# Kernel tuning notes

Measured on AMD Instinct MI355X. Metric: run time of the kernel, lower is better.

## Reference

```python
import jax, jax.numpy as jnp
import numpy as np

B, S, E, A = 4, 2048, 1024, 1024


def setup_inputs() -> dict:
    key = jax.random.key(0)
    k0, k1, k2, k3 = jax.random.split(key, 4)
    scale = 1.0 / np.sqrt(E)
    return {
        "embeds": jax.random.normal(k0, (B, S, E), dtype=jnp.float32),
        "Wq": jax.random.normal(k1, (E, A), dtype=jnp.float32) * scale,
        "Wk": jax.random.normal(k2, (E, A), dtype=jnp.float32) * scale,
        "Wv": jax.random.normal(k3, (E, A), dtype=jnp.float32) * scale,
    }


def reference(embeds, Wq, Wk, Wv):
    # projections: [B, S, A]
    q = jnp.einsum("bse,ea->bsa", embeds, Wq)
    k = jnp.einsum("bse,ea->bsa", embeds, Wk)
    v = jnp.einsum("bse,ea->bsa", embeds, Wv)
    attn_dim = k.shape[-1]
    # scores: [B, S, S], scaled by sqrt(attention_dim)
    scores = jnp.einsum("bqa,bka->bqk", q, k) / jnp.sqrt(
        jnp.asarray(attn_dim, dtype=q.dtype)
    )
    seq = scores.shape[-1]
    causal = jnp.tril(jnp.ones((seq, seq), dtype=bool))  # [S, S]
    scores = jnp.where(causal[None, :, :], scores, -jnp.inf)
    probs = jax.nn.softmax(scores, axis=-1)
    return jnp.einsum("bqk,bka->bqa", probs, v)
```

## Files before the change

kernel.cpp:

```cpp
#include <hip/hip_runtime.h>
#include <hip/hip_bf16.h>

#define DI __device__ __forceinline__

typedef __attribute__((ext_vector_type(8))) __bf16 bf16x8;
typedef __attribute__((ext_vector_type(4))) float f32x4;
typedef __attribute__((ext_vector_type(8))) short short8;
typedef __attribute__((ext_vector_type(4))) short short4v;
typedef unsigned short u16;

static constexpr int BB = 4, SS = 2048, EE = 1024, AA = 1024;

DI float bf2f(u16 u) { unsigned v = ((unsigned)u) << 16; float f; __builtin_memcpy(&f, &v, 4); return f; }
DI u16 f2bf(float f) { __hip_bfloat16 h = __float2bfloat16(f); u16 u; __builtin_memcpy(&u, &h, 2); return u; }

DI void gload16(const void* g, void* l) {
  __builtin_amdgcn_global_load_lds((const __attribute__((address_space(1))) void*)g,
                                   (__attribute__((address_space(3))) void*)l, 16, 0, 0);
}

DI int xcd_swz(int lin, int nwg) {
  int cpx = nwg >> 3;
  return (lin & 7) * cpx + (lin >> 3);
}

DI bf16x8 read_frag(const char* lds, int R, int c) {
  return *(const bf16x8*)(lds + R * 128 + ((c ^ (R & 7)) << 4));
}

DI void stage_tile(const u16* g, int ld, char* lds, int wid, int lane) {
#pragma unroll
  for (int i = 0; i < 4; ++i) {
    int blk = i * 4 + wid;
    int r = blk * 8 + (lane >> 3);
    int c = (lane & 7) ^ (r & 7);
    gload16((const char*)(g + (size_t)r * ld) + c * 16, lds + blk * 1024);
  }
}

DI void gemm_tile(const u16* Ap, int lda, const u16* Bp, int ldb, int ksteps,
                  char* smem, f32x4 acc[4][4]) {
  const int tid = threadIdx.x, lane = tid & 63, wid = tid >> 6;
  const int wr = wid >> 1, wc = wid & 1;
  stage_tile(Ap, lda, smem, wid, lane);
  stage_tile(Bp, ldb, smem + 16384, wid, lane);
  asm volatile("s_waitcnt vmcnt(0)" ::: "memory");
  __syncthreads();
#pragma unroll 1
  for (int ks = 0; ks < ksteps; ++ks) {
    const char* As = smem + (ks & 1) * 32768;
    const char* Bs = As + 16384;
    char* nxt = smem + ((ks & 1) ^ 1) * 32768;
    if (ks + 1 < ksteps) {
      stage_tile(Ap + (size_t)(ks + 1) * 64, lda, nxt, wid, lane);
      stage_tile(Bp + (size_t)(ks + 1) * 64, ldb, nxt + 16384, wid, lane);
    }
#pragma unroll
    for (int ksub = 0; ksub < 2; ++ksub) {
      const int c = ksub * 4 + (lane >> 4);
      bf16x8 af[4], bfr[4];
#pragma unroll
      for (int mi = 0; mi < 4; ++mi) af[mi] = read_frag(As, wr * 64 + mi * 16 + (lane & 15), c);
#pragma unroll
      for (int ni = 0; ni < 4; ++ni) bfr[ni] = read_frag(Bs, wc * 64 + ni * 16 + (lane & 15), c);
#pragma unroll
      for (int mi = 0; mi < 4; ++mi)
#pragma unroll
        for (int ni = 0; ni < 4; ++ni)
          acc[mi][ni] = __builtin_amdgcn_mfma_f32_16x16x32_bf16(af[mi], bfr[ni], acc[mi][ni], 0, 0, 0);
    }
    if (ks + 1 < ksteps) asm volatile("s_waitcnt vmcnt(0)" ::: "memory");
    __syncthreads();
  }
}

__global__ __launch_bounds__(256) void k_proj8(const u16* __restrict__ Xb, const u16* __restrict__ Wt,
                                               u16* __restrict__ Qb, u16* __restrict__ Vt) {
  __shared__ __align__(16) char smem[65536];
  const int lin = blockIdx.x;
  const int x = lin & 7;
  const int jj = lin >> 3;
  const int nh = jj / 96, rem = jj - nh * 96;
  const int nt = nh * 12 + (rem >> 3);
  const int mt = x * 8 + (rem & 7);
  const u16* Ap = Xb + (size_t)mt * 128 * EE;
  const u16* Bp = Wt + (size_t)nt * 128 * EE;
  f32x4 acc[4][4];
#pragma unroll
  for (int p = 0; p < 4; ++p)
#pragma unroll
    for (int q = 0; q < 4; ++q) acc[p][q] = (f32x4)0.f;
  gemm_tile(Ap, EE, Bp, EE, EE / 64, smem, acc);

  const int lane = threadIdx.x & 63, wid = threadIdx.x >> 6;
  const int lane15 = lane & 15, lhi = lane >> 4;
  const int wr = wid >> 1, wc = wid & 1;
  const int r0 = mt * 128 + wr * 64;
  const int c0 = nt * 128 + wc * 64;
  if (nt < 16) {
    u16* base = Qb + (size_t)(nt >> 3) * ((size_t)BB * SS * AA);
    const int cc = c0 & 1023;
#pragma unroll
    for (int mi = 0; mi < 4; ++mi)
#pragma unroll
      for (int ni = 0; ni < 4; ++ni)
#pragma unroll
        for (int r = 0; r < 4; ++r) {
          int row = r0 + mi * 16 + lhi * 4 + r;
          base[(size_t)row * AA + cc + ni * 16 + lane15] = f2bf(acc[mi][ni][r]);
        }
  } else {
#pragma unroll
    for (int mi = 0; mi < 4; ++mi) {
      const int grow = r0 + mi * 16 + lhi * 4;
      const int b = grow >> 11, s = grow & 2047;
#pragma unroll
      for (int ni = 0; ni < 4; ++ni) {
        const int a = c0 - 2048 + ni * 16 + lane15;
        short4v o;
#pragma unroll
        for (int r = 0; r < 4; ++r) o[r] = (short)f2bf(acc[mi][ni][r]);
        *(short4v*)(Vt + (size_t)b * AA * SS + (size_t)a * SS + s) = o;
      }
    }
  }
}

__global__ __launch_bounds__(256) void k_prep(const float* __restrict__ X, const float* __restrict__ Wq,
                                              const float* __restrict__ Wk, const float* __restrict__ Wv,
                                              u16* __restrict__ Xb, u16* __restrict__ Wt,
                                              float* __restrict__ rowsum) {
  __shared__ float t[64][65];
  const int bid = blockIdx.x;
  if (bid < 8192) {
    if (bid < 32) rowsum[bid * 256 + threadIdx.x] = 0.f;
    size_t i = ((size_t)bid * 256 + threadIdx.x) * 4;
    f32x4 f = *(const f32x4*)(X + i);
    short4v o;
#pragma unroll
    for (int j = 0; j < 4; ++j) o[j] = (short)f2bf(f[j]);
    *(short4v*)(Xb + i) = o;
  } else {
    const int bx = bid - 8192;
    const int w = bx >> 8, rem = bx & 255;
    const int k0 = (rem & 15) * 64, n0 = (rem >> 4) * 64;
    const float* W = (w == 0) ? Wq : ((w == 1) ? Wk : Wv);
    u16* Wo = Wt + (size_t)w * EE * AA;
    const int tx = threadIdx.x & 63, ty = threadIdx.x >> 6;
#pragma unroll
    for (int r = 0; r < 16; ++r) {
      int k = r * 4 + ty;
      t[k][tx] = W[(size_t)(k0 + k) * AA + n0 + tx];
    }
    __syncthreads();
#pragma unroll
    for (int r = 0; r < 16; ++r) {
      int n = r * 4 + ty;
      Wo[(size_t)(n0 + n) * EE + k0 + tx] = f2bf(t[tx][n]);
    }
  }
}

__global__ __launch_bounds__(256) void k_scores(const u16* __restrict__ Q, const u16* __restrict__ K,
                                                u16* __restrict__ Sc, float* __restrict__ rowsum) {
  __shared__ __align__(16) char smem[65536];
  const int wg = xcd_swz(blockIdx.x, 544);
  const int b = wg / 136, t = wg % 136;
  int i = (int)((sqrtf(8.f * t + 1.f) - 1.f) * 0.5f);
  while ((i + 1) * (i + 2) / 2 <= t) ++i;
  while (i * (i + 1) / 2 > t) --i;
  const int j = t - i * (i + 1) / 2;
  const u16* Ap = Q + (size_t)b * SS * AA + (size_t)i * 128 * AA;
  const u16* Bp = K + (size_t)b * SS * AA + (size_t)j * 128 * AA;
  u16* Op = Sc + (size_t)b * SS * SS;
  float* rs = rowsum + (size_t)b * SS;
  f32x4 acc[4][4];
#pragma unroll
  for (int p = 0; p < 4; ++p)
#pragma unroll
    for (int q = 0; q < 4; ++q) acc[p][q] = (f32x4)0.f;
  gemm_tile(Ap, AA, Bp, AA, AA / 64, smem, acc);
  const int lane = threadIdx.x & 63, wid = threadIdx.x >> 6;
  const int r0 = i * 128 + (wid >> 1) * 64, c0 = j * 128 + (wid & 1) * 64;
#pragma unroll
  for (int mi = 0; mi < 4; ++mi)
#pragma unroll
    for (int r = 0; r < 4; ++r) {
      const int row = r0 + mi * 16 + ((lane >> 4) << 2) + r;
      float psum = 0.f;
#pragma unroll
      for (int ni = 0; ni < 4; ++ni) {
        const int col = c0 + ni * 16 + (lane & 15);
        float e = (col <= row) ? __expf(acc[mi][ni][r] * 0.03125f) : 0.f;
        psum += e;
        Op[(size_t)row * SS + col] = f2bf(e);
      }
      psum += __shfl_xor(psum, 1, 16);
      psum += __shfl_xor(psum, 2, 16);
      psum += __shfl_xor(psum, 4, 16);
      psum += __shfl_xor(psum, 8, 16);
      if ((lane & 15) == 0) atomicAdd(&rs[row], psum);
    }
}

__global__ __launch_bounds__(256) void k_pv(const u16* __restrict__ Sc, const u16* __restrict__ Vt,
                                            const float* __restrict__ rowsum, float* __restrict__ Out) {
  __shared__ __align__(16) char smem[65536];
  const int lin = blockIdx.x;
  const int x = lin & 7;
  const int half = (lin >> 8) & 1;
  const int rest = (lin >> 3) & 31;
  const int b = rest >> 3, nt = rest & 7;
  const int i = half ? (15 - x) : x;
  const u16* Ap = Sc + (size_t)b * SS * SS + (size_t)i * 128 * SS;
  const u16* Bp = Vt + (size_t)b * AA * SS + (size_t)nt * 128 * SS;
  const float* rs = rowsum + (size_t)b * SS;
  float* Op = Out + (size_t)b * SS * AA;
  f32x4 acc[4][4];
#pragma unroll
  for (int p = 0; p < 4; ++p)
#pragma unroll
    for (int q = 0; q < 4; ++q) acc[p][q] = (f32x4)0.f;
  gemm_tile(Ap, SS, Bp, SS, 2 * (i + 1), smem, acc);
  const int lane = threadIdx.x & 63, wid = threadIdx.x >> 6;
  const int r0 = i * 128 + (wid >> 1) * 64, c0 = nt * 128 + (wid & 1) * 64;
#pragma unroll
  for (int mi = 0; mi < 4; ++mi)
#pragma unroll
    for (int r = 0; r < 4; ++r) {
      const int row = r0 + mi * 16 + ((lane >> 4) << 2) + r;
      const float inv = 1.f / rs[row];
#pragma unroll
      for (int ni = 0; ni < 4; ++ni) {
        const int col = c0 + ni * 16 + (lane & 15);
        Op[(size_t)row * AA + col] = acc[mi][ni][r] * inv;
      }
    }
}

extern "C" void kernel_launch(void* const* d_in, const int* in_sizes, int n_in,
                              void* d_out, int out_size, void* d_ws, size_t ws_size,
                              hipStream_t stream) {
  const float* X  = (const float*)d_in[0];
  const float* Wq = (const float*)d_in[1];
  const float* Wk = (const float*)d_in[2];
  const float* Wv = (const float*)d_in[3];
  float* Out = (float*)d_out;
  char* ws = (char*)d_ws;
  u16* Xb = (u16*)ws;
  u16* Wt = (u16*)(ws + (16u << 20));
  u16* Qb = (u16*)(ws + (22u << 20));
  u16* Kb = (u16*)(ws + (38u << 20));
  u16* Vt = (u16*)(ws + (70u << 20));
  u16* Sc = (u16*)(ws + (86u << 20));
  float* rowsum = (float*)(ws + (118u << 20));
  (void)Kb;

  k_prep<<<dim3(8192 + 768), 256, 0, stream>>>(X, Wq, Wk, Wv, Xb, Wt, rowsum);
  k_proj8<<<dim3(1536), 256, 0, stream>>>(Xb, Wt, Qb, Vt);
  k_scores<<<dim3(136 * BB), 256, 0, stream>>>(Qb, Kb, Sc, rowsum);
  k_pv<<<dim3(512), 256, 0, stream>>>(Sc, Vt, rowsum, Out);
}
```

Baseline: 139.8 us.

## Loop projection over three N tiles per block and reduce rowsum atomics in LDS

The projection kernel now launches 512 blocks, and each block computes three N-tiles in sequence instead of one per block. The aim is to cut launch and scheduling overhead and keep the A tile warm in cache. The prep conversion now handles 8 elements per thread. The scores kernel first accumulates row sums in shared memory and then does one global atomic per row, which cuts global atomic traffic. The PV kernel loads the row sums before the GEMM so their latency is hidden. The risk is fewer blocks (512 on a large GPU), which lowers parallelism and latency hiding in the projection.

```diff
diff --git a/kernel.cpp b/kernel.cpp
--- a/kernel.cpp
+++ b/kernel.cpp
@@ -74,53 +74,57 @@
   }
 }
 
-__global__ __launch_bounds__(256) void k_proj8(const u16* __restrict__ Xb, const u16* __restrict__ Wt,
+__global__ __launch_bounds__(256) void k_proj9(const u16* __restrict__ Xb, const u16* __restrict__ Wt,
                                                u16* __restrict__ Qb, u16* __restrict__ Vt) {
   __shared__ __align__(16) char smem[65536];
   const int lin = blockIdx.x;
   const int x = lin & 7;
   const int jj = lin >> 3;
-  const int nh = jj / 96, rem = jj - nh * 96;
-  const int nt = nh * 12 + (rem >> 3);
-  const int mt = x * 8 + (rem & 7);
+  const int mt = x * 8 + (jj & 7);
+  const int nb = jj >> 3;
   const u16* Ap = Xb + (size_t)mt * 128 * EE;
-  const u16* Bp = Wt + (size_t)nt * 128 * EE;
-  f32x4 acc[4][4];
-#pragma unroll
-  for (int p = 0; p < 4; ++p)
-#pragma unroll
-    for (int q = 0; q < 4; ++q) acc[p][q] = (f32x4)0.f;
-  gemm_tile(Ap, EE, Bp, EE, EE / 64, smem, acc);
-
   const int lane = threadIdx.x & 63, wid = threadIdx.x >> 6;
   const int lane15 = lane & 15, lhi = lane >> 4;
   const int wr = wid >> 1, wc = wid & 1;
-  const int r0 = mt * 128 + wr * 64;
-  const int c0 = nt * 128 + wc * 64;
-  if (nt < 16) {
-    u16* base = Qb + (size_t)(nt >> 3) * ((size_t)BB * SS * AA);
-    const int cc = c0 & 1023;
-#pragma unroll
-    for (int mi = 0; mi < 4; ++mi)
-#pragma unroll
-      for (int ni = 0; ni < 4; ++ni)
-#pragma unroll
-        for (int r = 0; r < 4; ++r) {
-          int row = r0 + mi * 16 + lhi * 4 + r;
-          base[(size_t)row * AA + cc + ni * 16 + lane15] = f2bf(acc[mi][ni][r]);
+
+#pragma unroll 1
+  for (int t3 = 0; t3 < 3; ++t3) {
+    const int nt = nb + t3 * 8;
+    const u16* Bp = Wt + (size_t)nt * 128 * EE;
+    f32x4 acc[4][4];
+#pragma unroll
+    for (int p = 0; p < 4; ++p)
+#pragma unroll
+      for (int q = 0; q < 4; ++q) acc[p][q] = (f32x4)0.f;
+    gemm_tile(Ap, EE, Bp, EE, EE / 64, smem, acc);
+
+    const int r0 = mt * 128 + wr * 64;
+    const int c0 = nt * 128 + wc * 64;
+    if (nt < 16) {
+      u16* base = Qb + (size_t)(nt >> 3) * ((size_t)BB * SS * AA);
+      const int cc = c0 & 1023;
+#pragma unroll
+      for (int mi = 0; mi < 4; ++mi)
+#pragma unroll
+        for (int ni = 0; ni < 4; ++ni)
+#pragma unroll
+          for (int r = 0; r < 4; ++r) {
+            int row = r0 + mi * 16 + lhi * 4 + r;
+            base[(size_t)row * AA + cc + ni * 16 + lane15] = f2bf(acc[mi][ni][r]);
+          }
+    } else {
+#pragma unroll
+      for (int mi = 0; mi < 4; ++mi) {
+        const int grow = r0 + mi * 16 + lhi * 4;
+        const int b = grow >> 11, s = grow & 2047;
+#pragma unroll
+        for (int ni = 0; ni < 4; ++ni) {
+          const int a = c0 - 2048 + ni * 16 + lane15;
+          short4v o;
+#pragma unroll
+          for (int r = 0; r < 4; ++r) o[r] = (short)f2bf(acc[mi][ni][r]);
+          *(short4v*)(Vt + (size_t)b * AA * SS + (size_t)a * SS + s) = o;
         }
-  } else {
-#pragma unroll
-    for (int mi = 0; mi < 4; ++mi) {
-      const int grow = r0 + mi * 16 + lhi * 4;
-      const int b = grow >> 11, s = grow & 2047;
-#pragma unroll
-      for (int ni = 0; ni < 4; ++ni) {
-        const int a = c0 - 2048 + ni * 16 + lane15;
-        short4v o;
-#pragma unroll
-        for (int r = 0; r < 4; ++r) o[r] = (short)f2bf(acc[mi][ni][r]);
-        *(short4v*)(Vt + (size_t)b * AA * SS + (size_t)a * SS + s) = o;
       }
     }
   }
@@ -132,16 +136,17 @@
                                               float* __restrict__ rowsum) {
   __shared__ float t[64][65];
   const int bid = blockIdx.x;
-  if (bid < 8192) {
+  if (bid < 4096) {
     if (bid < 32) rowsum[bid * 256 + threadIdx.x] = 0.f;
-    size_t i = ((size_t)bid * 256 + threadIdx.x) * 4;
-    f32x4 f = *(const f32x4*)(X + i);
-    short4v o;
-#pragma unroll
-    for (int j = 0; j < 4; ++j) o[j] = (short)f2bf(f[j]);
-    *(short4v*)(Xb + i) = o;
+    size_t i = ((size_t)bid * 256 + threadIdx.x) * 8;
+    f32x4 f0 = *(const f32x4*)(X + i);
+    f32x4 f1 = *(const f32x4*)(X + i + 4);
+    short8 o;
+#pragma unroll
+    for (int j = 0; j < 4; ++j) { o[j] = (short)f2bf(f0[j]); o[4 + j] = (short)f2bf(f1[j]); }
+    *(short8*)(Xb + i) = o;
   } else {
-    const int bx = bid - 8192;
+    const int bx = bid - 4096;
     const int w = bx >> 8, rem = bx & 255;
     const int k0 = (rem & 15) * 64, n0 = (rem >> 4) * 64;
     const float* W = (w == 0) ? Wq : ((w == 1) ? Wk : Wv);
@@ -164,6 +169,7 @@
 __global__ __launch_bounds__(256) void k_scores(const u16* __restrict__ Q, const u16* __restrict__ K,
                                                 u16* __restrict__ Sc, float* __restrict__ rowsum) {
   __shared__ __align__(16) char smem[65536];
+  __shared__ float rsh[128];
   const int wg = xcd_swz(blockIdx.x, 544);
   const int b = wg / 136, t = wg % 136;
   int i = (int)((sqrtf(8.f * t + 1.f) - 1.f) * 0.5f);
@@ -179,6 +185,7 @@
   for (int p = 0; p < 4; ++p)
 #pragma unroll
     for (int q = 0; q < 4; ++q) acc[p][q] = (f32x4)0.f;
+  if (threadIdx.x < 128) rsh[threadIdx.x] = 0.f;
   gemm_tile(Ap, AA, Bp, AA, AA / 64, smem, acc);
   const int lane = threadIdx.x & 63, wid = threadIdx.x >> 6;
   const int r0 = i * 128 + (wid >> 1) * 64, c0 = j * 128 + (wid & 1) * 64;
@@ -199,8 +206,10 @@
       psum += __shfl_xor(psum, 2, 16);
       psum += __shfl_xor(psum, 4, 16);
       psum += __shfl_xor(psum, 8, 16);
-      if ((lane & 15) == 0) atomicAdd(&rs[row], psum);
-    }
+      if ((lane & 15) == 0) atomicAdd(&rsh[row - i * 128], psum);
+    }
+  __syncthreads();
+  if (threadIdx.x < 128) atomicAdd(&rs[i * 128 + threadIdx.x], rsh[threadIdx.x]);
 }
 
 __global__ __launch_bounds__(256) void k_pv(const u16* __restrict__ Sc, const u16* __restrict__ Vt,
@@ -216,20 +225,26 @@
   const u16* Bp = Vt + (size_t)b * AA * SS + (size_t)nt * 128 * SS;
   const float* rs = rowsum + (size_t)b * SS;
   float* Op = Out + (size_t)b * SS * AA;
+  const int lane = threadIdx.x & 63, wid = threadIdx.x >> 6;
+  const int r0 = i * 128 + (wid >> 1) * 64, c0 = nt * 128 + (wid & 1) * 64;
+  float rsv[4][4];
+#pragma unroll
+  for (int mi = 0; mi < 4; ++mi)
+#pragma unroll
+    for (int r = 0; r < 4; ++r)
+      rsv[mi][r] = rs[r0 + mi * 16 + ((lane >> 4) << 2) + r];
   f32x4 acc[4][4];
 #pragma unroll
   for (int p = 0; p < 4; ++p)
 #pragma unroll
     for (int q = 0; q < 4; ++q) acc[p][q] = (f32x4)0.f;
   gemm_tile(Ap, SS, Bp, SS, 2 * (i + 1), smem, acc);
-  const int lane = threadIdx.x & 63, wid = threadIdx.x >> 6;
-  const int r0 = i * 128 + (wid >> 1) * 64, c0 = nt * 128 + (wid & 1) * 64;
 #pragma unroll
   for (int mi = 0; mi < 4; ++mi)
 #pragma unroll
     for (int r = 0; r < 4; ++r) {
       const int row = r0 + mi * 16 + ((lane >> 4) << 2) + r;
-      const float inv = 1.f / rs[row];
+      const float inv = 1.f / rsv[mi][r];
 #pragma unroll
       for (int ni = 0; ni < 4; ++ni) {
         const int col = c0 + ni * 16 + (lane & 15);
@@ -254,10 +269,9 @@
   u16* Vt = (u16*)(ws + (70u << 20));
   u16* Sc = (u16*)(ws + (86u << 20));
   float* rowsum = (float*)(ws + (118u << 20));
-  (void)Kb;
-
-  k_prep<<<dim3(8192 + 768), 256, 0, stream>>>(X, Wq, Wk, Wv, Xb, Wt, rowsum);
-  k_proj8<<<dim3(1536), 256, 0, stream>>>(Xb, Wt, Qb, Vt);
+
+  k_prep<<<dim3(4096 + 768), 256, 0, stream>>>(X, Wq, Wk, Wv, Xb, Wt, rowsum);
+  k_proj9<<<dim3(512), 256, 0, stream>>>(Xb, Wt, Qb, Vt);
   k_scores<<<dim3(136 * BB), 256, 0, stream>>>(Qb, Kb, Sc, rowsum);
   k_pv<<<dim3(512), 256, 0, stream>>>(Sc, Vt, rowsum, Out);
 }
```

Result: slower. 146.7 us (+4.9%).
